# Optimization experiments

Measured on AMD Instinct MI355X. Metric: run time of the kernel, lower is better.

The kernel has to match this reference:

```python
import jax, jax.numpy as jnp
import numpy as np

N, D, F, E, K = 16384, 512, 2048, 8, 2


def setup_inputs() -> dict:
    key = jax.random.key(0)
    ks = jax.random.split(key, 5)
    s = 0.02
    return {
        "x": jax.random.normal(ks[0], (N, D), dtype=jnp.float32),
        "gate_w": jax.random.normal(ks[1], (D, E), dtype=jnp.float32) * s,
        "w1": jax.random.normal(ks[2], (E, D, F), dtype=jnp.float32) * s,
        "w2": jax.random.normal(ks[3], (E, F, D), dtype=jnp.float32) * s,
        "w3": jax.random.normal(ks[4], (E, D, F), dtype=jnp.float32) * s,
    }


def reference(x, gate_w, w1, w2, w3):
    # gate: [N, E] logits -> top-k experts per token
    logits = x @ gate_w
    top_vals, top_idx = jax.lax.top_k(logits, K)          # [N, K]
    # softmax over the selected-k logits in float32 (matches F.softmax dtype=float)
    weights = jax.nn.softmax(top_vals.astype(jnp.float32), axis=-1).astype(x.dtype)
    out = jnp.zeros_like(x)
    for e in range(E):
        # combine weight for expert e per token (0 if not selected)
        m = jnp.sum(jnp.where(top_idx == e, weights, 0.0), axis=-1)  # [N]
        h = jax.nn.silu(x @ w1[e]) * (x @ w3[e])                     # [N, F]
        out = out + m[:, None] * (h @ w2[e])
    return out
```

## Files before the change

kernel.cpp:

```cpp
#include <hip/hip_runtime.h>
#include <hip/hip_bf16.h>
#include <math.h>

#define N_TOK 16384
#define DIM   512
#define FDIM  2048
#define NEXP  8
#define TOPK  2
#define PAIRS (N_TOK*TOPK)
#define MAX_TILES (PAIRS/128 + NEXP)

typedef __hip_bfloat16 bf16;
typedef __attribute__((ext_vector_type(8))) short bf16x8;
typedef __attribute__((ext_vector_type(4))) float f32x4;
typedef __attribute__((ext_vector_type(8))) short s16x8;

__device__ __forceinline__ short f2bf(float f){
  union { float f; unsigned u; } v; v.f = f;
  unsigned r = v.u + 0x7fffu + ((v.u >> 16) & 1u);
  return (short)(r >> 16);
}
__device__ __forceinline__ float bf2f(short s){
  union { unsigned u; float f; } v; v.u = ((unsigned)(unsigned short)s) << 16;
  return v.f;
}
__device__ __forceinline__ void g2l16(const void* g, void* l){
  __builtin_amdgcn_global_load_lds(
      (const __attribute__((address_space(1))) unsigned int*)g,
      (__attribute__((address_space(3))) unsigned int*)l, 16, 0, 0);
}

__global__ __launch_bounds__(512) void k_gate(const float* __restrict__ x,
    const float* __restrict__ gw, int* __restrict__ tidx, float* __restrict__ tw){
  __shared__ float gwT[NEXP][DIM];
  int tid = threadIdx.x;
  #pragma unroll
  for(int i=0;i<8;i++){
    int idx = tid + 512*i;
    gwT[idx&7][idx>>3] = gw[idx];
  }
  __syncthreads();
  int lane = tid & 63, wid = tid >> 6;
  int t = blockIdx.x*8 + wid;
  const float* xr = x + (size_t)t*DIM;
  float acc[NEXP];
  #pragma unroll
  for(int e=0;e<NEXP;e++) acc[e]=0.f;
  #pragma unroll
  for(int c=0;c<8;c++){
    float xv = xr[c*64 + lane];
    #pragma unroll
    for(int e=0;e<NEXP;e++) acc[e] += xv * gwT[e][c*64+lane];
  }
  #pragma unroll
  for(int off=32; off; off>>=1){
    #pragma unroll
    for(int e=0;e<NEXP;e++) acc[e] += __shfl_xor(acc[e], off);
  }
  if(lane==0){
    int e0=0; float v0=acc[0];
    #pragma unroll
    for(int e=1;e<NEXP;e++) if(acc[e]>v0){v0=acc[e]; e0=e;}
    int e1=-1; float v1=-1e30f;
    #pragma unroll
    for(int e=0;e<NEXP;e++) if(e!=e0 && acc[e]>v1){v1=acc[e]; e1=e;}
    float z = expf(v1-v0);
    float w0 = 1.f/(1.f+z);
    tidx[t*2]=e0; tidx[t*2+1]=e1;
    tw[t*2]=w0; tw[t*2+1]=1.f-w0;
  }
}

__global__ __launch_bounds__(256) void k_count(const int* __restrict__ tidx,
                                               int* __restrict__ counts){
  __shared__ int h[NEXP];
  if(threadIdx.x<NEXP) h[threadIdx.x]=0;
  __syncthreads();
  int i0 = blockIdx.x*1024 + threadIdx.x;
  #pragma unroll
  for(int k=0;k<4;k++) atomicAdd(&h[tidx[i0 + 256*k]], 1);
  __syncthreads();
  if(threadIdx.x<NEXP) atomicAdd(&counts[threadIdx.x], h[threadIdx.x]);
}

__global__ void k_route(const int* __restrict__ counts, int* __restrict__ offsets,
    int* __restrict__ ntiles, int* __restrict__ te, int* __restrict__ tb,
    int* __restrict__ ts){
  if(threadIdx.x==0){
    int off=0, nt=0;
    for(int e=0;e<NEXP;e++){
      offsets[e]=off;
      int c=counts[e];
      int tiles=(c+127)>>7;
      for(int i=0;i<tiles;i++){ te[nt]=e; tb[nt]=off+(i<<7); ts[nt]=off+c; nt++; }
      off += c;
    }
    *ntiles=nt;
  }
}

__global__ __launch_bounds__(256) void k_scatter(const int* __restrict__ tidx,
    const int* __restrict__ offsets, int* __restrict__ fill,
    int* __restrict__ token_list, int* __restrict__ posmap){
  __shared__ int lcnt[NEXP], lbase[NEXP];
  if(threadIdx.x<NEXP) lcnt[threadIdx.x]=0;
  __syncthreads();
  int i = blockIdx.x*256 + threadIdx.x;
  int e = tidx[i];
  int rank = atomicAdd(&lcnt[e], 1);
  __syncthreads();
  if(threadIdx.x<NEXP) lbase[threadIdx.x] = atomicAdd(&fill[threadIdx.x], lcnt[threadIdx.x]);
  __syncthreads();
  int pos = offsets[e] + lbase[e] + rank;
  token_list[pos] = i>>1;
  posmap[i] = pos;
}

__global__ __launch_bounds__(256) void k_cast(const float* __restrict__ x,
                                              bf16* __restrict__ xb){
  int i = blockIdx.x*256 + threadIdx.x;
  const float* p = x + (size_t)i*8;
  f32x4 a = *(const f32x4*)p;
  f32x4 b = *(const f32x4*)(p+4);
  s16x8 r;
  r[0]=f2bf(a[0]); r[1]=f2bf(a[1]); r[2]=f2bf(a[2]); r[3]=f2bf(a[3]);
  r[4]=f2bf(b[0]); r[5]=f2bf(b[1]); r[6]=f2bf(b[2]); r[7]=f2bf(b[3]);
  *(s16x8*)((short*)xb + (size_t)i*8) = r;
}

__global__ __launch_bounds__(256) void k_transpose(const float* __restrict__ src,
    bf16* __restrict__ dst, int R, int C){
  __shared__ float tile[32][33];
  const float* s = src + (size_t)blockIdx.z*R*C;
  short* d = (short*)dst + (size_t)blockIdx.z*R*C;
  int c0 = blockIdx.x*32, r0 = blockIdx.y*32;
  int tx = threadIdx.x & 31, ty = threadIdx.x >> 5;
  #pragma unroll
  for(int i=0;i<4;i++) tile[ty+8*i][tx] = s[(size_t)(r0+ty+8*i)*C + c0+tx];
  __syncthreads();
  #pragma unroll
  for(int i=0;i<4;i++) d[(size_t)(c0+ty+8*i)*R + r0+tx] = f2bf(tile[tx][ty+8*i]);
}

__global__ __launch_bounds__(256,3) void k_gemmA(const bf16* __restrict__ xb,
    const bf16* __restrict__ w1T, const bf16* __restrict__ w3T,
    const int* __restrict__ ntiles, const int* __restrict__ te,
    const int* __restrict__ tb, const int* __restrict__ ts,
    const int* __restrict__ token_list, bf16* __restrict__ H){
  int tile = blockIdx.x;
  if(tile >= *ntiles) return;
  int e = te[tile], base = tb[tile], send = ts[tile];
  int f0 = blockIdx.y*64;
  __shared__ short As[128*32];
  __shared__ short B1s[64*32];
  __shared__ short B3s[64*32];
  int tid = threadIdx.x;
  int srow0 = tid>>2, srow1 = 64 + (tid>>2), scol = (tid&3)*8;
  int r0g = base + srow0, r1g = base + srow1;
  int tok0 = token_list[(r0g < send) ? r0g : base];
  int tok1 = token_list[(r1g < send) ? r1g : base];
  const short* gA0 = (const short*)xb + (size_t)tok0*DIM + scol;
  const short* gA1 = (const short*)xb + (size_t)tok1*DIM + scol;
  const short* gB1 = (const short*)w1T + ((size_t)e*FDIM + f0 + srow0)*DIM + scol;
  const short* gB3 = (const short*)w3T + ((size_t)e*FDIM + f0 + srow0)*DIM + scol;
  char* lA  = (char*)As  + tid*16;
  char* lB1 = (char*)B1s + tid*16;
  char* lB3 = (char*)B3s + tid*16;
  int wid = tid>>6, lane = tid&63;
  int wr = wid>>1, wc = wid&1;
  int lrow = lane&15, lk = (lane>>4)<<3;
  f32x4 acc1[4][2] = {};
  f32x4 acc3[4][2] = {};
  for(int d0=0; d0<DIM; d0+=32){
    __syncthreads();
    g2l16(gA0 + d0, lA);
    g2l16(gA1 + d0, lA + 4096);
    g2l16(gB1 + d0, lB1);
    g2l16(gB3 + d0, lB3);
    __syncthreads();
    bf16x8 af[4], b1f[2], b3f[2];
    #pragma unroll
    for(int m=0;m<4;m++) af[m] = *(const bf16x8*)&As[(wr*64+m*16+lrow)*32 + lk];
    #pragma unroll
    for(int n=0;n<2;n++){ b1f[n] = *(const bf16x8*)&B1s[(wc*32+n*16+lrow)*32 + lk];
                          b3f[n] = *(const bf16x8*)&B3s[(wc*32+n*16+lrow)*32 + lk]; }
    #pragma unroll
    for(int m=0;m<4;m++){
      #pragma unroll
      for(int n=0;n<2;n++){
        acc1[m][n] = __builtin_amdgcn_mfma_f32_16x16x32_bf16(af[m], b1f[n], acc1[m][n], 0,0,0);
        acc3[m][n] = __builtin_amdgcn_mfma_f32_16x16x32_bf16(af[m], b3f[n], acc3[m][n], 0,0,0);
      }
    }
  }
  #pragma unroll
  for(int m=0;m<4;m++){
    int r0 = base + wr*64 + m*16 + ((lane>>4)<<2);
    #pragma unroll
    for(int n=0;n<2;n++){
      int col = f0 + wc*32 + n*16 + lrow;
      #pragma unroll
      for(int j=0;j<4;j++){
        if(r0+j < send){
          float a = acc1[m][n][j];
          float h = a * (1.f/(1.f+__expf(-a))) * acc3[m][n][j];
          ((short*)H)[(size_t)(r0+j)*FDIM + col] = f2bf(h);
        }
      }
    }
  }
}

__global__ __launch_bounds__(256,3) void k_gemmB(const bf16* __restrict__ H,
    const bf16* __restrict__ w2T, const int* __restrict__ ntiles,
    const int* __restrict__ te, const int* __restrict__ tb,
    const int* __restrict__ ts, bf16* __restrict__ O){
  int tile = blockIdx.x;
  if(tile >= *ntiles) return;
  int e = te[tile], base = tb[tile], send = ts[tile];
  int n0 = blockIdx.y*64;
  __shared__ short As[128*32];
  __shared__ short Bs[64*32];
  int tid = threadIdx.x;
  int srow0 = tid>>2, srow1 = 64 + (tid>>2), scol = (tid&3)*8;
  int r0g = base + srow0, r1g = base + srow1;
  int ar0 = (r0g < send) ? r0g : base;
  int ar1 = (r1g < send) ? r1g : base;
  const short* gA0 = (const short*)H + (size_t)ar0*FDIM + scol;
  const short* gA1 = (const short*)H + (size_t)ar1*FDIM + scol;
  const short* gB  = (const short*)w2T + ((size_t)e*DIM + n0 + srow0)*FDIM + scol;
  char* lA = (char*)As + tid*16;
  char* lB = (char*)Bs + tid*16;
  int wid = tid>>6, lane = tid&63, wr = wid>>1, wc = wid&1;
  int lrow = lane&15, lk = (lane>>4)<<3;
  f32x4 acc[4][2] = {};
  for(int k0=0; k0<FDIM; k0+=32){
    __syncthreads();
    g2l16(gA0 + k0, lA);
    g2l16(gA1 + k0, lA + 4096);
    g2l16(gB  + k0, lB);
    __syncthreads();
    bf16x8 af[4], bfr[2];
    #pragma unroll
    for(int m=0;m<4;m++) af[m]  = *(const bf16x8*)&As[(wr*64+m*16+lrow)*32 + lk];
    #pragma unroll
    for(int n=0;n<2;n++) bfr[n] = *(const bf16x8*)&Bs[(wc*32+n*16+lrow)*32 + lk];
    #pragma unroll
    for(int m=0;m<4;m++){
      #pragma unroll
      for(int n=0;n<2;n++)
        acc[m][n] = __builtin_amdgcn_mfma_f32_16x16x32_bf16(af[m], bfr[n], acc[m][n], 0,0,0);
    }
  }
  #pragma unroll
  for(int m=0;m<4;m++){
    #pragma unroll
    for(int j=0;j<4;j++){
      int r2 = base + wr*64 + m*16 + ((lane>>4)<<2) + j;
      if(r2 < send){
        #pragma unroll
        for(int n=0;n<2;n++){
          int col = n0 + wc*32 + n*16 + lrow;
          ((short*)O)[(size_t)r2*DIM + col] = f2bf(acc[m][n][j]);
        }
      }
    }
  }
}

__global__ __launch_bounds__(256) void k_combine(const bf16* __restrict__ O,
    const int* __restrict__ posmap, const float* __restrict__ tw,
    float* __restrict__ out){
  int lane = threadIdx.x & 63, wid = threadIdx.x >> 6;
  int t = blockIdx.x*4 + wid;
  int p0 = posmap[2*t], p1 = posmap[2*t+1];
  float w0 = tw[2*t], w1 = tw[2*t+1];
  s16x8 a = *(const s16x8*)((const short*)O + (size_t)p0*DIM + lane*8);
  s16x8 b = *(const s16x8*)((const short*)O + (size_t)p1*DIM + lane*8);
  f32x4 r0, r1;
  #pragma unroll
  for(int j=0;j<4;j++) r0[j] = w0*bf2f(a[j]) + w1*bf2f(b[j]);
  #pragma unroll
  for(int j=0;j<4;j++) r1[j] = w0*bf2f(a[4+j]) + w1*bf2f(b[4+j]);
  float* o = out + (size_t)t*DIM + lane*8;
  *(f32x4*)o = r0;
  *(f32x4*)(o+4) = r1;
}

extern "C" void kernel_launch(void* const* d_in, const int* in_sizes, int n_in,
                              void* d_out, int out_size, void* d_ws, size_t ws_size,
                              hipStream_t stream){
  const float* x  = (const float*)d_in[0];
  const float* gw = (const float*)d_in[1];
  const float* w1 = (const float*)d_in[2];
  const float* w2 = (const float*)d_in[3];
  const float* w3 = (const float*)d_in[4];
  float* out = (float*)d_out;
  char* ws = (char*)d_ws;

  int* cw = (int*)ws;
  int* counts = cw;
  int* fill   = cw + 8;
  int* offsets= cw + 16;
  int* ntiles = cw + 24;
  int* te = cw + 32;
  int* tb = cw + 296;
  int* ts = cw + 560;
  int* tidx       = cw + 824;
  int* token_list = cw + 824 + PAIRS;
  int* posmap     = cw + 824 + 2*PAIRS;
  float* tw       = (float*)(cw + 824 + 3*PAIRS);

  const size_t MB = 1u<<20;
  bf16* xb  = (bf16*)(ws + 1*MB);
  bf16* w1T = (bf16*)(ws + 17*MB);
  bf16* w3T = (bf16*)(ws + 33*MB);
  bf16* w2T = (bf16*)(ws + 49*MB);
  bf16* Hbuf= (bf16*)(ws + 65*MB);
  bf16* Obuf= (bf16*)(ws + 17*MB);
  size_t needed = 65*MB + (size_t)PAIRS*FDIM*2u;
  if(ws_size < needed) return;

  hipMemsetAsync(d_ws, 0, 64, stream);

  k_gate<<<N_TOK/8, 512, 0, stream>>>(x, gw, tidx, tw);
  k_count<<<PAIRS/1024, 256, 0, stream>>>(tidx, counts);
  k_route<<<1, 64, 0, stream>>>(counts, offsets, ntiles, te, tb, ts);
  k_scatter<<<PAIRS/256, 256, 0, stream>>>(tidx, offsets, fill, token_list, posmap);
  k_cast<<<(N_TOK*DIM/8)/256, 256, 0, stream>>>(x, xb);
  k_transpose<<<dim3(FDIM/32, DIM/32, NEXP), 256, 0, stream>>>(w1, w1T, DIM, FDIM);
  k_transpose<<<dim3(FDIM/32, DIM/32, NEXP), 256, 0, stream>>>(w3, w3T, DIM, FDIM);
  k_transpose<<<dim3(DIM/32, FDIM/32, NEXP), 256, 0, stream>>>(w2, w2T, FDIM, DIM);
  k_gemmA<<<dim3(MAX_TILES, FDIM/64), 256, 0, stream>>>(xb, w1T, w3T, ntiles, te, tb, ts, token_list, Hbuf);
  k_gemmB<<<dim3(MAX_TILES, DIM/64), 256, 0, stream>>>(Hbuf, w2T, ntiles, te, tb, ts, Obuf);
  k_combine<<<N_TOK/4, 256, 0, stream>>>(Obuf, posmap, tw, out);
}
```

Measured before the change: 589.8 us.

## Double-buffer LDS tiles with XOR swizzle in both expert GEMMs, widen gemmB N-tile

Both grouped GEMM kernels now double-buffer their shared-memory tiles, so the global-to-LDS copy for the next K-slice is issued while MFMAs run on the current one. This halves the barriers per iteration. The shared-memory column index is XOR-swizzled to reduce bank conflicts on fragment reads. gemmB's output tile grows from 64 to 128 columns, raising reuse of the A (H) tile and halving the grid. The cost is more LDS and accumulator registers per block, which may lower occupancy.

```diff
diff --git a/kernel.cpp b/kernel.cpp
--- a/kernel.cpp
+++ b/kernel.cpp
@@ -151,11 +151,13 @@
   if(tile >= *ntiles) return;
   int e = te[tile], base = tb[tile], send = ts[tile];
   int f0 = blockIdx.y*64;
-  __shared__ short As[128*32];
-  __shared__ short B1s[64*32];
-  __shared__ short B3s[64*32];
+  __shared__ short As[2*128*32];
+  __shared__ short B1s[2*64*32];
+  __shared__ short B3s[2*64*32];
   int tid = threadIdx.x;
-  int srow0 = tid>>2, srow1 = 64 + (tid>>2), scol = (tid&3)*8;
+  int srow0 = tid>>2, srow1 = 64 + (tid>>2);
+  int sx = (tid>>3)&3;
+  int scol = ((tid&3) ^ sx)*8;
   int r0g = base + srow0, r1g = base + srow1;
   int tok0 = token_list[(r0g < send) ? r0g : base];
   int tok1 = token_list[(r1g < send) ? r1g : base];
@@ -163,27 +165,45 @@
   const short* gA1 = (const short*)xb + (size_t)tok1*DIM + scol;
   const short* gB1 = (const short*)w1T + ((size_t)e*FDIM + f0 + srow0)*DIM + scol;
   const short* gB3 = (const short*)w3T + ((size_t)e*FDIM + f0 + srow0)*DIM + scol;
-  char* lA  = (char*)As  + tid*16;
-  char* lB1 = (char*)B1s + tid*16;
-  char* lB3 = (char*)B3s + tid*16;
+  char* dA  = (char*)As  + tid*16;
+  char* dB1 = (char*)B1s + tid*16;
+  char* dB3 = (char*)B3s + tid*16;
   int wid = tid>>6, lane = tid&63;
   int wr = wid>>1, wc = wid&1;
-  int lrow = lane&15, lk = (lane>>4)<<3;
+  int lrow = lane&15, g = lane>>4;
   f32x4 acc1[4][2] = {};
   f32x4 acc3[4][2] = {};
-  for(int d0=0; d0<DIM; d0+=32){
-    __syncthreads();
-    g2l16(gA0 + d0, lA);
-    g2l16(gA1 + d0, lA + 4096);
-    g2l16(gB1 + d0, lB1);
-    g2l16(gB3 + d0, lB3);
-    __syncthreads();
+  g2l16(gA0, dA);
+  g2l16(gA1, dA + 4096);
+  g2l16(gB1, dB1);
+  g2l16(gB3, dB3);
+  __syncthreads();
+  int p = 0;
+  for(int t=0; t<16; t++){
+    if(t<15){
+      int d1 = (t+1)*32;
+      int ao = (p^1)*8192, bo = (p^1)*4096;
+      g2l16(gA0 + d1, dA + ao);
+      g2l16(gA1 + d1, dA + ao + 4096);
+      g2l16(gB1 + d1, dB1 + bo);
+      g2l16(gB3 + d1, dB3 + bo);
+    }
+    const short* Ab  = As  + p*4096;
+    const short* B1b = B1s + p*2048;
+    const short* B3b = B3s + p*2048;
     bf16x8 af[4], b1f[2], b3f[2];
     #pragma unroll
-    for(int m=0;m<4;m++) af[m] = *(const bf16x8*)&As[(wr*64+m*16+lrow)*32 + lk];
-    #pragma unroll
-    for(int n=0;n<2;n++){ b1f[n] = *(const bf16x8*)&B1s[(wc*32+n*16+lrow)*32 + lk];
-                          b3f[n] = *(const bf16x8*)&B3s[(wc*32+n*16+lrow)*32 + lk]; }
+    for(int m=0;m<4;m++){
+      int r = wr*64 + m*16 + lrow;
+      af[m] = *(const bf16x8*)&Ab[r*32 + ((g ^ ((r>>1)&3))<<3)];
+    }
+    #pragma unroll
+    for(int n=0;n<2;n++){
+      int r = wc*32 + n*16 + lrow;
+      int c = (g ^ ((r>>1)&3))<<3;
+      b1f[n] = *(const bf16x8*)&B1b[r*32 + c];
+      b3f[n] = *(const bf16x8*)&B3b[r*32 + c];
+    }
     #pragma unroll
     for(int m=0;m<4;m++){
       #pragma unroll
@@ -192,6 +212,8 @@
         acc3[m][n] = __builtin_amdgcn_mfma_f32_16x16x32_bf16(af[m], b3f[n], acc3[m][n], 0,0,0);
       }
     }
+    __syncthreads();
+    p ^= 1;
   }
   #pragma unroll
   for(int m=0;m<4;m++){
@@ -218,39 +240,61 @@
   int tile = blockIdx.x;
   if(tile >= *ntiles) return;
   int e = te[tile], base = tb[tile], send = ts[tile];
-  int n0 = blockIdx.y*64;
-  __shared__ short As[128*32];
-  __shared__ short Bs[64*32];
+  int n0 = blockIdx.y*128;
+  __shared__ short As[2*128*32];
+  __shared__ short Bs[2*128*32];
   int tid = threadIdx.x;
-  int srow0 = tid>>2, srow1 = 64 + (tid>>2), scol = (tid&3)*8;
+  int srow0 = tid>>2, srow1 = 64 + (tid>>2);
+  int sx = (tid>>3)&3;
+  int scol = ((tid&3) ^ sx)*8;
   int r0g = base + srow0, r1g = base + srow1;
   int ar0 = (r0g < send) ? r0g : base;
   int ar1 = (r1g < send) ? r1g : base;
   const short* gA0 = (const short*)H + (size_t)ar0*FDIM + scol;
   const short* gA1 = (const short*)H + (size_t)ar1*FDIM + scol;
-  const short* gB  = (const short*)w2T + ((size_t)e*DIM + n0 + srow0)*FDIM + scol;
-  char* lA = (char*)As + tid*16;
-  char* lB = (char*)Bs + tid*16;
+  const short* gB0 = (const short*)w2T + ((size_t)e*DIM + n0 + srow0)*FDIM + scol;
+  const short* gB1 = (const short*)w2T + ((size_t)e*DIM + n0 + srow1)*FDIM + scol;
+  char* dA = (char*)As + tid*16;
+  char* dB = (char*)Bs + tid*16;
   int wid = tid>>6, lane = tid&63, wr = wid>>1, wc = wid&1;
-  int lrow = lane&15, lk = (lane>>4)<<3;
-  f32x4 acc[4][2] = {};
-  for(int k0=0; k0<FDIM; k0+=32){
-    __syncthreads();
-    g2l16(gA0 + k0, lA);
-    g2l16(gA1 + k0, lA + 4096);
-    g2l16(gB  + k0, lB);
-    __syncthreads();
-    bf16x8 af[4], bfr[2];
-    #pragma unroll
-    for(int m=0;m<4;m++) af[m]  = *(const bf16x8*)&As[(wr*64+m*16+lrow)*32 + lk];
-    #pragma unroll
-    for(int n=0;n<2;n++) bfr[n] = *(const bf16x8*)&Bs[(wc*32+n*16+lrow)*32 + lk];
+  int lrow = lane&15, g = lane>>4;
+  f32x4 acc[4][4] = {};
+  g2l16(gA0, dA);
+  g2l16(gA1, dA + 4096);
+  g2l16(gB0, dB);
+  g2l16(gB1, dB + 4096);
+  __syncthreads();
+  int p = 0;
+  for(int t=0; t<64; t++){
+    if(t<63){
+      int d1 = (t+1)*32;
+      int o = (p^1)*8192;
+      g2l16(gA0 + d1, dA + o);
+      g2l16(gA1 + d1, dA + o + 4096);
+      g2l16(gB0 + d1, dB + o);
+      g2l16(gB1 + d1, dB + o + 4096);
+    }
+    const short* Ab = As + p*4096;
+    const short* Bb = Bs + p*4096;
+    bf16x8 af[4], bfr[4];
+    #pragma unroll
+    for(int m=0;m<4;m++){
+      int r = wr*64 + m*16 + lrow;
+      af[m] = *(const bf16x8*)&Ab[r*32 + ((g ^ ((r>>1)&3))<<3)];
+    }
+    #pragma unroll
+    for(int n=0;n<4;n++){
+      int r = wc*64 + n*16 + lrow;
+      bfr[n] = *(const bf16x8*)&Bb[r*32 + ((g ^ ((r>>1)&3))<<3)];
+    }
     #pragma unroll
     for(int m=0;m<4;m++){
       #pragma unroll
-      for(int n=0;n<2;n++)
+      for(int n=0;n<4;n++)
         acc[m][n] = __builtin_amdgcn_mfma_f32_16x16x32_bf16(af[m], bfr[n], acc[m][n], 0,0,0);
     }
+    __syncthreads();
+    p ^= 1;
   }
   #pragma unroll
   for(int m=0;m<4;m++){
@@ -259,8 +303,8 @@
       int r2 = base + wr*64 + m*16 + ((lane>>4)<<2) + j;
       if(r2 < send){
         #pragma unroll
-        for(int n=0;n<2;n++){
-          int col = n0 + wc*32 + n*16 + lrow;
+        for(int n=0;n<4;n++){
+          int col = n0 + wc*64 + n*16 + lrow;
           ((short*)O)[(size_t)r2*DIM + col] = f2bf(acc[m][n][j]);
         }
       }
@@ -332,6 +376,6 @@
   k_transpose<<<dim3(FDIM/32, DIM/32, NEXP), 256, 0, stream>>>(w3, w3T, DIM, FDIM);
   k_transpose<<<dim3(DIM/32, FDIM/32, NEXP), 256, 0, stream>>>(w2, w2T, FDIM, DIM);
   k_gemmA<<<dim3(MAX_TILES, FDIM/64), 256, 0, stream>>>(xb, w1T, w3T, ntiles, te, tb, ts, token_list, Hbuf);
-  k_gemmB<<<dim3(MAX_TILES, DIM/64), 256, 0, stream>>>(Hbuf, w2T, ntiles, te, tb, ts, Obuf);
+  k_gemmB<<<dim3(MAX_TILES, DIM/128), 256, 0, stream>>>(Hbuf, w2T, ntiles, te, tb, ts, Obuf);
   k_combine<<<N_TOK/4, 256, 0, stream>>>(Obuf, posmap, tw, out);
 }
```

New measurement: 511.6 us. 1.15x faster.
